# Optimization experiments

Measured on AMD Instinct MI355X. Metric: run time of the kernel, lower is better.

## Reference

```python
import jax, jax.numpy as jnp
import numpy as np

D_DIM = 128
K_DIM = 32


def setup_inputs() -> dict:
    key = jax.random.key(0)
    k1, k2, k3 = jax.random.split(key, 3)
    B, H, W = 8, 64, 64
    std1 = 1.0 / (K_DIM * D_DIM) ** 0.5
    std2 = 1.0 / K_DIM ** 0.5
    X = jax.random.normal(k1, (B, D_DIM, H, W), dtype=jnp.float32)
    codewords = jax.random.uniform(k2, (K_DIM, D_DIM), dtype=jnp.float32, minval=-std1, maxval=std1)
    scale = jax.random.uniform(k3, (K_DIM,), dtype=jnp.float32, minval=-std2, maxval=std2)
    return {"X": X, "codewords": codewords, "scale": scale}


def reference(X, codewords, scale):
    # X: [B, D, H, W] -> descriptors [B, N, D]
    B, D, H, W = X.shape
    Xf = X.reshape(B, D, H * W).transpose(0, 2, 1)  # [B, N, D]
    # Squared distance ||x - c||^2 expanded: avoids materializing [B,N,K,D]
    x_sq = jnp.sum(Xf * Xf, axis=-1, keepdims=True)          # [B, N, 1]
    c_sq = jnp.sum(codewords * codewords, axis=-1)           # [K]
    cross = jnp.einsum('bnd,kd->bnk', Xf, codewords)         # [B, N, K]
    dist2 = x_sq - 2.0 * cross + c_sq                        # [B, N, K]
    # NOTE: faithful to source -- softmax over scale * dist^2 (no negation)
    A = jax.nn.softmax(dist2 * scale, axis=-1)               # [B, N, K]
    # E[b,k,d] = sum_n A[b,n,k] * (x[b,n,d] - c[k,d])
    E = jnp.einsum('bnk,bnd->bkd', A, Xf) - jnp.sum(A, axis=1)[..., None] * codewords
    return E  # [B, K, D]
```

## Files before the change

kernel.cpp:

```cpp
#include <hip/hip_runtime.h>
#include <hip/hip_bf16.h>

#define D_DIM 128
#define K_DIM 32
#define NPIX  4096
#define TPB   128

typedef __bf16 bf16x8 __attribute__((ext_vector_type(8)));
typedef unsigned short u16x8 __attribute__((ext_vector_type(8)));
typedef float f32x4 __attribute__((ext_vector_type(4)));

__device__ __forceinline__ unsigned short f2bf(float f) {
    union { float f; unsigned u; } v; v.f = f;
    unsigned r = v.u + 0x7FFFu + ((v.u >> 16) & 1u);
    return (unsigned short)(r >> 16);
}
__device__ __forceinline__ unsigned pack2(float lo, float hi) {
    __hip_bfloat162 h = __float22bfloat162_rn(make_float2(lo, hi));
    union { __hip_bfloat162 b; unsigned u; } u; u.b = h;
    return u.u;
}
__device__ __forceinline__ float bf2f(unsigned short u) {
    union { unsigned u; float f; } v; v.u = ((unsigned)u) << 16;
    return v.f;
}
__device__ __forceinline__ bf16x8 ldfrag(const unsigned short* p) {
    union { u16x8 s; bf16x8 b; } u;
    u.s = *(const u16x8*)p;
    return u.b;
}
__device__ __forceinline__ bf16x8 pack8(float4 a, float4 b) {
    union { unsigned d[4]; bf16x8 v; } u;
    u.d[0] = pack2(a.x, a.y); u.d[1] = pack2(a.z, a.w);
    u.d[2] = pack2(b.x, b.y); u.d[3] = pack2(b.z, b.w);
    return u.v;
}

#define XND_LD 136
#define CW_LD  136
#define SA_LD  136

__global__ __launch_bounds__(512) void enc_kernel(
    const float* __restrict__ X,
    const float* __restrict__ cw,
    const float* __restrict__ scale,
    float* __restrict__ out)
{
    __shared__ __align__(16) unsigned short sXnd[TPB * XND_LD];
    __shared__ __align__(16) unsigned short sCW[K_DIM * CW_LD];
    __shared__ __align__(16) unsigned short sA[K_DIM * SA_LD];
    __shared__ float sXsqP[16 * 129];
    __shared__ float sXsq[TPB];
    __shared__ float sSum[K_DIM];
    __shared__ float sSc[K_DIM];
    __shared__ float sCS[K_DIM];

    const int ltid = threadIdx.x;
    const int b    = blockIdx.x >> 5;
    const int n0   = (blockIdx.x & 31) * TPB;
    const int lane = ltid & 63;
    const int w    = ltid >> 6;
    const int l15  = lane & 15;
    const int quad = lane >> 4;

    if (ltid < K_DIM) {
        const float4* cr = (const float4*)(cw + ltid * D_DIM);
        float cs = 0.f;
        #pragma unroll 8
        for (int q = 0; q < 32; ++q) {
            float4 c4 = cr[q];
            cs = fmaf(c4.x, c4.x, fmaf(c4.y, c4.y, fmaf(c4.z, c4.z, fmaf(c4.w, c4.w, cs))));
        }
        float s = scale[ltid];
        sSc[ltid] = s;
        sCS[ltid] = cs * s;
        sSum[ltid] = 0.f;
    }

    {
        const int r  = ltid >> 4;
        const int q8 = ltid & 15;
        float4 c0 = *(const float4*)(cw + r * D_DIM + 8 * q8);
        float4 c1 = *(const float4*)(cw + r * D_DIM + 8 * q8 + 4);
        uint4 pk;
        pk.x = pack2(c0.x, c0.y); pk.y = pack2(c0.z, c0.w);
        pk.z = pack2(c1.x, c1.y); pk.w = pack2(c1.z, c1.w);
        *(uint4*)&sCW[r * CW_LD + 8 * q8] = pk;
    }

    {
        const int c   = ltid & 15;
        const int rp  = (ltid >> 4) & 3;
        const int ph  = ltid >> 6;
        const int pxh = (ph & 1) * 64;
        const int dbl = (ph >> 1) * 16;
        float px[4] = {0.f, 0.f, 0.f, 0.f};
        const float* xb = X + (size_t)b * D_DIM * NPIX + n0 + pxh;
        #pragma unroll
        for (int p = 0; p < 4; ++p) {
            const int pair = rp + 4 * p + dbl;
            const int d0   = 2 * pair;
            float4 f0 = *(const float4*)(xb + (size_t)d0 * NPIX + 4 * c);
            float4 f1 = *(const float4*)(xb + (size_t)(d0 + 1) * NPIX + 4 * c);
            px[0] = fmaf(f0.x, f0.x, fmaf(f1.x, f1.x, px[0]));
            px[1] = fmaf(f0.y, f0.y, fmaf(f1.y, f1.y, px[1]));
            px[2] = fmaf(f0.z, f0.z, fmaf(f1.z, f1.z, px[2]));
            px[3] = fmaf(f0.w, f0.w, fmaf(f1.w, f1.w, px[3]));
            const int pix = pxh + 4 * c;
            *(unsigned*)&sXnd[(pix + 0) * XND_LD + d0] = pack2(f0.x, f1.x);
            *(unsigned*)&sXnd[(pix + 1) * XND_LD + d0] = pack2(f0.y, f1.y);
            *(unsigned*)&sXnd[(pix + 2) * XND_LD + d0] = pack2(f0.z, f1.z);
            *(unsigned*)&sXnd[(pix + 3) * XND_LD + d0] = pack2(f0.w, f1.w);
        }
        const int row = rp + 4 * (ph >> 1);
        #pragma unroll
        for (int j = 0; j < 4; ++j) sXsqP[row * 129 + pxh + 4 * c + j] = px[j];
    }

    float4 g[4][2];
    {
        const int d = 16 * w + l15;
        const float* xrow = X + ((size_t)b * D_DIM + d) * NPIX + n0;
        #pragma unroll
        for (int ks = 0; ks < 4; ++ks) {
            const float* p = xrow + 8 * quad + 32 * ks;
            g[ks][0] = *(const float4*)p;
            g[ks][1] = *(const float4*)(p + 4);
        }
    }
    __syncthreads();

    if (ltid < TPB) {
        float s = 0.f;
        #pragma unroll
        for (int r = 0; r < 16; ++r) s += sXsqP[r * 129 + ltid];
        sXsq[ltid] = s;
    }

    f32x4 accA[2] = {{0.f, 0.f, 0.f, 0.f}, {0.f, 0.f, 0.f, 0.f}};
    {
        const int prow = (16 * w + l15) * XND_LD;
        #pragma unroll
        for (int ks = 0; ks < 4; ++ks) {
            const int off = 8 * quad + 32 * ks;
            bf16x8 bfrag = ldfrag(&sXnd[prow + off]);
            bf16x8 a0 = ldfrag(&sCW[l15 * CW_LD + off]);
            bf16x8 a1 = ldfrag(&sCW[(l15 + 16) * CW_LD + off]);
            accA[0] = __builtin_amdgcn_mfma_f32_16x16x32_bf16(a0, bfrag, accA[0], 0, 0, 0);
            accA[1] = __builtin_amdgcn_mfma_f32_16x16x32_bf16(a1, bfrag, accA[1], 0, 0, 0);
        }
    }
    __syncthreads();

    {
        const float xsq = sXsq[16 * w + l15];
        float e8[8];
        float psum = 0.f;
        #pragma unroll
        for (int mt = 0; mt < 2; ++mt)
            #pragma unroll
            for (int reg = 0; reg < 4; ++reg) {
                const int k = 16 * mt + 4 * quad + reg;
                float l = fmaf(sSc[k], fmaf(-2.f, accA[mt][reg], xsq), sCS[k]);
                float e = __expf(l);
                e8[4 * mt + reg] = e;
                psum += e;
            }
        psum += __shfl_xor(psum, 16);
        psum += __shfl_xor(psum, 32);
        const float inv = 1.f / psum;
        float r8[8];
        #pragma unroll
        for (int i = 0; i < 8; ++i) {
            e8[i] *= inv;
            r8[i] = e8[i];
        }
        #pragma unroll
        for (int mt = 0; mt < 2; ++mt)
            #pragma unroll
            for (int reg = 0; reg < 4; ++reg) {
                const int k = 16 * mt + 4 * quad + reg;
                sA[k * SA_LD + 16 * w + l15] = f2bf(e8[4 * mt + reg]);
            }
        #pragma unroll
        for (int i = 0; i < 8; ++i) {
            r8[i] += __shfl_xor(r8[i], 1);
            r8[i] += __shfl_xor(r8[i], 2);
            r8[i] += __shfl_xor(r8[i], 4);
            r8[i] += __shfl_xor(r8[i], 8);
        }
        if (l15 == 0) {
            #pragma unroll
            for (int mt = 0; mt < 2; ++mt)
                #pragma unroll
                for (int reg = 0; reg < 4; ++reg)
                    atomicAdd(&sSum[16 * mt + 4 * quad + reg], r8[4 * mt + reg]);
        }
    }
    __syncthreads();

    f32x4 accE[2] = {{0.f, 0.f, 0.f, 0.f}, {0.f, 0.f, 0.f, 0.f}};
    {
        #pragma unroll
        for (int ks = 0; ks < 4; ++ks) {
            const int off = 8 * quad + 32 * ks;
            bf16x8 bfrag = pack8(g[ks][0], g[ks][1]);
            bf16x8 a0 = ldfrag(&sA[l15 * SA_LD + off]);
            bf16x8 a1 = ldfrag(&sA[(l15 + 16) * SA_LD + off]);
            accE[0] = __builtin_amdgcn_mfma_f32_16x16x32_bf16(a0, bfrag, accE[0], 0, 0, 0);
            accE[1] = __builtin_amdgcn_mfma_f32_16x16x32_bf16(a1, bfrag, accE[1], 0, 0, 0);
        }
    }

    {
        float* outb = out + (size_t)b * (K_DIM * D_DIM);
        const int d = 16 * w + l15;
        #pragma unroll
        for (int mt = 0; mt < 2; ++mt) {
            #pragma unroll
            for (int rr = 0; rr < 4; ++rr) {
                const int reg = (rr + blockIdx.x) & 3;
                const int k = 16 * mt + 4 * quad + reg;
                float sk  = sSum[k];
                float cwv = bf2f(sCW[k * CW_LD + d]);
                float v = fmaf(-sk, cwv, accE[mt][reg]);
                atomicAdd(outb + k * D_DIM + d, v);
            }
        }
    }
}

extern "C" void kernel_launch(void* const* d_in, const int* in_sizes, int n_in,
                              void* d_out, int out_size, void* d_ws, size_t ws_size,
                              hipStream_t stream) {
    const float* X  = (const float*)d_in[0];
    const float* cw = (const float*)d_in[1];
    const float* sc = (const float*)d_in[2];
    float* out = (float*)d_out;
    (void)in_sizes; (void)n_in; (void)d_ws; (void)ws_size; (void)out_size;

    hipLaunchKernelGGL(enc_kernel, dim3(256), dim3(512), 0, stream, X, cw, sc, out);
}
```

Before: 72.05 us.

## Replace global atomic accumulation with per-block partials and a reduce kernel

Each block now writes its partial E tile to workspace instead of doing atomicAdd into the output. A second kernel sums the 32 partials per batch into the output. The goal is to remove contention from 32 blocks atomically adding to the same output rows. In exchange it adds a kernel launch and about 4 MB of workspace traffic. It also makes the result deterministic and no longer depends on the output being zeroed beforehand.

New measurement: 73.31 us. No clear change (+1.7%).

```diff
diff --git a/kernel.cpp b/kernel.cpp
--- a/kernel.cpp
+++ b/kernel.cpp
@@ -44,7 +44,7 @@
     const float* __restrict__ X,
     const float* __restrict__ cw,
     const float* __restrict__ scale,
-    float* __restrict__ out)
+    float* __restrict__ ws)
 {
     __shared__ __align__(16) unsigned short sXnd[TPB * XND_LD];
     __shared__ __align__(16) unsigned short sCW[K_DIM * CW_LD];
@@ -213,21 +213,35 @@
     }
 
     {
-        float* outb = out + (size_t)b * (K_DIM * D_DIM);
+        float* wsl = ws + (size_t)blockIdx.x * (K_DIM * D_DIM);
         const int d = 16 * w + l15;
         #pragma unroll
         for (int mt = 0; mt < 2; ++mt) {
             #pragma unroll
-            for (int rr = 0; rr < 4; ++rr) {
-                const int reg = (rr + blockIdx.x) & 3;
+            for (int reg = 0; reg < 4; ++reg) {
                 const int k = 16 * mt + 4 * quad + reg;
                 float sk  = sSum[k];
                 float cwv = bf2f(sCW[k * CW_LD + d]);
-                float v = fmaf(-sk, cwv, accE[mt][reg]);
-                atomicAdd(outb + k * D_DIM + d, v);
+                wsl[k * D_DIM + d] = fmaf(-sk, cwv, accE[mt][reg]);
             }
         }
     }
+}
+
+__global__ __launch_bounds__(64) void reduce_kernel(
+    const float4* __restrict__ ws, float4* __restrict__ out)
+{
+    const int tid = blockIdx.x * 64 + threadIdx.x;
+    const int b   = tid >> 10;
+    const int r   = tid & 1023;
+    const float4* p = ws + (size_t)b * 32 * 1024 + r;
+    float4 s = make_float4(0.f, 0.f, 0.f, 0.f);
+    #pragma unroll
+    for (int t = 0; t < 32; ++t) {
+        float4 v = p[(size_t)t * 1024];
+        s.x += v.x; s.y += v.y; s.z += v.z; s.w += v.w;
+    }
+    out[tid] = s;
 }
 
 extern "C" void kernel_launch(void* const* d_in, const int* in_sizes, int n_in,
@@ -237,7 +251,10 @@
     const float* cw = (const float*)d_in[1];
     const float* sc = (const float*)d_in[2];
     float* out = (float*)d_out;
-    (void)in_sizes; (void)n_in; (void)d_ws; (void)ws_size; (void)out_size;
-
-    hipLaunchKernelGGL(enc_kernel, dim3(256), dim3(512), 0, stream, X, cw, sc, out);
-}
+    (void)in_sizes; (void)n_in; (void)ws_size; (void)out_size;
+
+    hipLaunchKernelGGL(enc_kernel, dim3(256), dim3(512), 0, stream,
+                       X, cw, sc, (float*)d_ws);
+    hipLaunchKernelGGL(reduce_kernel, dim3(128), dim3(64), 0, stream,
+                       (const float4*)d_ws, (float4*)out);
+}
```
